# Performance work log

Hardware: AMD Instinct MI355X
Metric: run time of the kernel (lower is better)

Reference implementation:

```python
import jax, jax.numpy as jnp
import numpy as np

N_NODES = 100000
N_EDGES = 1600000
N_FEAT = 128
N_HID = 128
N_CLASS = 10
N_GRAPHS = 512
BN_EPS = 1e-5


def setup_inputs() -> dict:
    key = jax.random.key(0)
    ks = jax.random.split(key, 12)
    x = jax.random.normal(ks[0], (N_NODES, N_FEAT), dtype=jnp.float32)
    edge_index = jax.random.randint(ks[1], (2, N_EDGES), 0, N_NODES, dtype=jnp.int32)
    batch = jnp.sort(jax.random.randint(ks[2], (N_NODES,), 0, N_GRAPHS, dtype=jnp.int32))
    s1 = 1.0 / np.sqrt(N_FEAT)
    s2 = 1.0 / np.sqrt(N_HID)
    W1 = jax.random.uniform(ks[3], (N_FEAT, N_HID), jnp.float32, -s1, s1)
    b1 = jax.random.uniform(ks[4], (N_HID,), jnp.float32, -s1, s1)
    gamma = jnp.ones((N_HID,), jnp.float32)
    beta = jnp.zeros((N_HID,), jnp.float32)
    W2 = jax.random.uniform(ks[5], (N_HID, N_HID), jnp.float32, -s2, s2)
    b2 = jax.random.uniform(ks[6], (N_HID,), jnp.float32, -s2, s2)
    clsW = jax.random.uniform(ks[7], (N_HID, N_CLASS), jnp.float32, -s2, s2)
    clsb = jax.random.uniform(ks[8], (N_CLASS,), jnp.float32, -s2, s2)
    return {"x": x, "edge_index": edge_index, "batch": batch,
            "W1": W1, "b1": b1, "gamma": gamma, "beta": beta,
            "W2": W2, "b2": b2, "clsW": clsW, "clsb": clsb}


def _gcn_norm(edge_index, n_nodes):
    # add self-loops, compute symmetric normalization D^-1/2 A_hat D^-1/2
    loops = jnp.arange(n_nodes, dtype=edge_index.dtype)
    src = jnp.concatenate([edge_index[0], loops])
    dst = jnp.concatenate([edge_index[1], loops])
    deg = jax.ops.segment_sum(jnp.ones_like(dst, dtype=jnp.float32), dst,
                              num_segments=n_nodes)
    dinv = jnp.where(deg > 0, jax.lax.rsqrt(deg), 0.0)
    norm = dinv[src] * dinv[dst]  # [E + N]
    return src, dst, norm


def _gcn_conv(h, src, dst, norm, W, b, n_nodes):
    h = h @ W                                   # [N, nhid] dense GEMM
    msg = h[src] * norm[:, None]                # gather + scale  [E+N, nhid]
    out = jax.ops.segment_sum(msg, dst, num_segments=n_nodes)  # scatter-add
    return out + b


def reference(x, edge_index, batch, W1, b1, gamma, beta, W2, b2, clsW, clsb):
    n_nodes = x.shape[0]
    src, dst, norm = _gcn_norm(edge_index, n_nodes)
    # layer 1: GCNConv -> BatchNorm(eval, running stats 0/1) -> ReLU -> Dropout(eval=id)
    h = _gcn_conv(x, src, dst, norm, W1, b1, n_nodes)
    h = h * (gamma / jnp.sqrt(1.0 + BN_EPS)) + beta
    h = jax.nn.relu(h)
    # layer 2: GCNConv (output layer, no bn/act)
    h = _gcn_conv(h, src, dst, norm, W2, b2, n_nodes)
    # global mean pool over batch index
    sums = jax.ops.segment_sum(h, batch, num_segments=N_GRAPHS)          # [G, nhid]
    cnts = jax.ops.segment_sum(jnp.ones((n_nodes,), h.dtype), batch,
                               num_segments=N_GRAPHS)
    g = sums / jnp.maximum(cnts, 1.0)[:, None]
    out = jax.nn.log_softmax(g @ clsW + clsb, axis=1)                    # [G, nclass]
    return out, g
```

## Files before the change

### kernel.cpp

```cpp
#include <hip/hip_runtime.h>
#include <hip/hip_bf16.h>

#define N_NODES 100000
#define N_EDGES 1600000
#define N_FEAT 128
#define N_HID 128
#define N_CLASS 10
#define N_GRAPHS 512
#define BN_RSQRT 0.9999950000374997f

#define NRANGE 12500
#define NSUB 512
#define SCAP 640
#define HGROUP 32
#define BPB (NSUB / HGROUP)

typedef _Float16 half_t;
typedef __attribute__((ext_vector_type(2))) _Float16 half2v;
typedef __attribute__((ext_vector_type(4))) _Float16 half4v;
typedef __attribute__((ext_vector_type(8))) _Float16 half8v;
typedef __attribute__((ext_vector_type(4))) float floatx4;
typedef __attribute__((ext_vector_type(2))) float floatx2;

__global__ __launch_bounds__(256) void bucket_fused(
    const int* __restrict__ src, const int* __restrict__ dst,
    int* __restrict__ cnt, unsigned long long* __restrict__ bucketed,
    const float* __restrict__ W1, half_t* __restrict__ Wt1,
    const float* __restrict__ W2, half_t* __restrict__ Wt2,
    const int* __restrict__ batch, int* __restrict__ boffs,
    int chunkE, int E, int nnodes)
{
    __shared__ int wcnt[4][8];
    __shared__ int wbase[4][8];
    int blk = blockIdx.x;
    if (blk >= NSUB) {
        int k = blk - NSUB;
        if (k < 128) {
            int i = k * 256 + threadIdx.x;
            const float* W = (i < 16384) ? W1 : W2;
            half_t* Wt = (i < 16384) ? Wt1 : Wt2;
            int j = i & 16383;
            int c = j >> 7, kk = j & 127;
            Wt[(size_t)c * 128 + kk] = (half_t)W[(size_t)kk * 128 + c];
        } else {
            int i = (k - 128) * 256 + threadIdx.x;
            if (i < nnodes) {
                int b = batch[i];
                int prev = (i == 0) ? -1 : batch[i - 1];
                for (int g = prev + 1; g <= b; ++g) boffs[g] = i;
                if (i == nnodes - 1)
                    for (int g = b + 1; g <= N_GRAPHS; ++g) boffs[g] = nnodes;
            }
        }
        return;
    }
    int b = blk;
    int wave = threadIdx.x >> 6;
    int lane = threadIdx.x & 63;
    int e0 = b * chunkE;
    int e1 = e0 + chunkE < E ? e0 + chunkE : E;
    int iters = (chunkE + 255) / 256;

    int mycnt = 0;
    for (int it = 0; it < iters; ++it) {
        int e = e0 + it * 256 + threadIdx.x;
        bool valid = e < e1;
        int d = valid ? dst[e] : 0;
        int rr = (d * 8) / N_NODES;
#pragma unroll
        for (int r = 0; r < 8; ++r) {
            unsigned long long m = __ballot(valid && rr == r);
            if (lane == r) mycnt += __popcll(m);
        }
    }
    if (lane < 8) wcnt[wave][lane] = mycnt;
    __syncthreads();
    if (threadIdx.x < 8) {
        int r = threadIdx.x;
        int s = 0;
#pragma unroll
        for (int w = 0; w < 4; ++w) { wbase[w][r] = s; s += wcnt[w][r]; }
        cnt[r * NSUB + b] = s;
    }
    __syncthreads();

    int myoff = (lane < 8) ? wbase[wave][lane] : 0;
    for (int it = 0; it < iters; ++it) {
        int e = e0 + it * 256 + threadIdx.x;
        bool valid = e < e1;
        int s = valid ? src[e] : 0;
        int d = valid ? dst[e] : 0;
        int rr = (d * 8) / N_NODES;
        unsigned long long pk = ((unsigned long long)(unsigned)d << 32) | (unsigned)s;
#pragma unroll
        for (int r = 0; r < 8; ++r) {
            unsigned long long m = __ballot(valid && rr == r);
            int base_r = __shfl(myoff, r);
            if (valid && rr == r) {
                int pos = base_r + __popcll(m & ((1ull << lane) - 1));
                if (pos < SCAP)
                    bucketed[(size_t)(r * NSUB + b) * SCAP + pos] = pk;
            }
            if (lane == r) myoff += __popcll(m);
        }
    }
}

__global__ __launch_bounds__(256) void hist2(
    const unsigned long long* __restrict__ bucketed, const int* __restrict__ cnt,
    int* __restrict__ partial)
{
    __shared__ int h[NRANGE];
    int r = blockIdx.x & 7, g = blockIdx.x >> 3;
    for (int i = threadIdx.x; i < NRANGE; i += 256) h[i] = 0;
    __syncthreads();
    int rbase = r * NRANGE;
    for (int j = 0; j < BPB; ++j) {
        int b = g * BPB + j;
        int n = cnt[r * NSUB + b];
        if (n > SCAP) n = SCAP;
        const unsigned long long* seg = bucketed + (size_t)(r * NSUB + b) * SCAP;
        for (int i = threadIdx.x; i < n; i += 256)
            atomicAdd(&h[(int)(seg[i] >> 32) - rbase], 1);
    }
    __syncthreads();
    int* slice = partial + (size_t)(r * HGROUP + g) * NRANGE;
    for (int i = threadIdx.x; i < NRANGE; i += 256) slice[i] = h[i];
}

__global__ void deg_reduce(const int* __restrict__ partial, int* __restrict__ deg,
                           float* __restrict__ dinv, int* __restrict__ bsums, int n) {
    __shared__ int sm[256];
    int t = threadIdx.x;
    int i = blockIdx.x * 256 + t;
    int s = 0;
    if (i < n) {
        int rr = i / NRANGE;
        int dl = i - rr * NRANGE;
        const int* p = partial + (size_t)rr * HGROUP * NRANGE + dl;
#pragma unroll 8
        for (int g = 0; g < HGROUP; ++g) s += p[(size_t)g * NRANGE];
        deg[i] = s;
        dinv[i] = rsqrtf((float)s + 1.0f);
    }
    sm[t] = s;
    __syncthreads();
    for (int off = 128; off > 0; off >>= 1) {
        if (t < off) sm[t] += sm[t + off];
        __syncthreads();
    }
    if (t == 0) bsums[blockIdx.x] = sm[0];
}

__global__ void scan_small(int* __restrict__ bsums, int nb) {
    __shared__ int buf[1024];
    int t = threadIdx.x;
    int v = (t < nb) ? bsums[t] : 0;
    buf[t] = v;
    __syncthreads();
    for (int off = 1; off < 1024; off <<= 1) {
        int x = (t >= off) ? buf[t - off] : 0;
        __syncthreads();
        buf[t] += x;
        __syncthreads();
    }
    if (t < nb) bsums[t] = buf[t] - v;
}

__global__ __launch_bounds__(256) void scan_chunkoff_gemm1(
    const int* __restrict__ in, const int* __restrict__ bsums,
    int* __restrict__ rowptr, int* __restrict__ partial,
    int n, int total, int nb,
    const float* __restrict__ X, const half_t* __restrict__ Wt,
    const float* __restrict__ dinv, unsigned char* __restrict__ Y8, int nrows)
{
    __shared__ int s[256];
    if (blockIdx.x < (unsigned)nb) {
        int t = threadIdx.x;
        int i = blockIdx.x * 256 + t;
        int v = (i < n) ? in[i] : 0;
        s[t] = v;
        __syncthreads();
        for (int off = 1; off < 256; off <<= 1) {
            int x = (t >= off) ? s[t - off] : 0;
            __syncthreads();
            s[t] += x;
            __syncthreads();
        }
        if (i == 0) rowptr[n] = total;
        if (i < n) {
            int excl = bsums[blockIdx.x] + s[t] - v;
            rowptr[i] = excl;
            int rr = i / NRANGE;
            int dl = i - rr * NRANGE;
            int* p = partial + (size_t)rr * HGROUP * NRANGE + dl;
            int running = excl;
            for (int g = 0; g < HGROUP; ++g) {
                int tmp = p[(size_t)g * NRANGE];
                p[(size_t)g * NRANGE] = running;
                running += tmp;
            }
        }
        return;
    }
    int bb = blockIdx.x - nb;
    int wave = threadIdx.x >> 6;
    int lane = threadIdx.x & 63;
    int n16  = lane & 15;
    int quad = lane >> 4;
    int r0 = bb * 64 + wave * 16;
    if (r0 >= nrows) return;
    int row = r0 + n16;
    const float4* xrow = (const float4*)(X + (size_t)row * 128);
    half8v a[4];
#pragma unroll
    for (int kc = 0; kc < 4; ++kc) {
        float4 f0 = xrow[kc * 8 + quad * 2];
        float4 f1 = xrow[kc * 8 + quad * 2 + 1];
        half8v t = {(half_t)f0.x, (half_t)f0.y, (half_t)f0.z, (half_t)f0.w,
                    (half_t)f1.x, (half_t)f1.y, (half_t)f1.z, (half_t)f1.w};
        a[kc] = t;
    }
    float dr = dinv[row];
#pragma unroll
    for (int c = 0; c < 8; ++c) {
        const half8v* wrow = (const half8v*)(Wt + (size_t)(c * 16 + n16) * 128);
        floatx4 acc = {0.f, 0.f, 0.f, 0.f};
        acc = __builtin_amdgcn_mfma_f32_16x16x32_f16(wrow[0 * 4 + quad], a[0], acc, 0, 0, 0);
        acc = __builtin_amdgcn_mfma_f32_16x16x32_f16(wrow[1 * 4 + quad], a[1], acc, 0, 0, 0);
        acc = __builtin_amdgcn_mfma_f32_16x16x32_f16(wrow[2 * 4 + quad], a[2], acc, 0, 0, 0);
        acc = __builtin_amdgcn_mfma_f32_16x16x32_f16(wrow[3 * 4 + quad], a[3], acc, 0, 0, 0);
        int packed = __builtin_amdgcn_cvt_pk_fp8_f32(acc[0] * dr, acc[1] * dr, 0, false);
        packed = __builtin_amdgcn_cvt_pk_fp8_f32(acc[2] * dr, acc[3] * dr, packed, true);
        *(int*)(Y8 + (size_t)row * 128 + c * 16 + quad * 4) = packed;
    }
}

__global__ __launch_bounds__(256) void fill2(
    const unsigned long long* __restrict__ bucketed, const int* __restrict__ cnt,
    const int* __restrict__ partial, int* __restrict__ col)
{
    __shared__ int off[NRANGE];
    int r = blockIdx.x & 7, g = blockIdx.x >> 3;
    const int* slice = partial + (size_t)(r * HGROUP + g) * NRANGE;
    for (int i = threadIdx.x; i < NRANGE; i += 256) off[i] = slice[i];
    __syncthreads();
    int rbase = r * NRANGE;
    for (int j = 0; j < BPB; ++j) {
        int b = g * BPB + j;
        int n = cnt[r * NSUB + b];
        if (n > SCAP) n = SCAP;
        const unsigned long long* seg = bucketed + (size_t)(r * NSUB + b) * SCAP;
        for (int i = threadIdx.x; i < n; i += 256) {
            unsigned long long pk = seg[i];
            int pos = atomicAdd(&off[(int)(pk >> 32) - rbase], 1);
            col[pos] = (int)((unsigned)(pk & 0xffffffffu) << 7);
        }
    }
}

__global__ __launch_bounds__(256) void gemm2_mfma(
    const half_t* __restrict__ X, const half_t* __restrict__ Wt,
    const float* __restrict__ dinv, unsigned char* __restrict__ Y8, int nrows)
{
    int wave = threadIdx.x >> 6;
    int lane = threadIdx.x & 63;
    int n16  = lane & 15;
    int quad = lane >> 4;
    int r0 = blockIdx.x * 64 + wave * 16;
    if (r0 >= nrows) return;
    int row = r0 + n16;
    const half8v* xrow = (const half8v*)(X + (size_t)row * 128);
    half8v a0 = xrow[0 * 4 + quad];
    half8v a1 = xrow[1 * 4 + quad];
    half8v a2 = xrow[2 * 4 + quad];
    half8v a3 = xrow[3 * 4 + quad];
    float dr = dinv[row];
#pragma unroll
    for (int c = 0; c < 8; ++c) {
        const half8v* wrow = (const half8v*)(Wt + (size_t)(c * 16 + n16) * 128);
        floatx4 acc = {0.f, 0.f, 0.f, 0.f};
        acc = __builtin_amdgcn_mfma_f32_16x16x32_f16(wrow[0 * 4 + quad], a0, acc, 0, 0, 0);
        acc = __builtin_amdgcn_mfma_f32_16x16x32_f16(wrow[1 * 4 + quad], a1, acc, 0, 0, 0);
        acc = __builtin_amdgcn_mfma_f32_16x16x32_f16(wrow[2 * 4 + quad], a2, acc, 0, 0, 0);
        acc = __builtin_amdgcn_mfma_f32_16x16x32_f16(wrow[3 * 4 + quad], a3, acc, 0, 0, 0);
        int packed = __builtin_amdgcn_cvt_pk_fp8_f32(acc[0] * dr, acc[1] * dr, 0, false);
        packed = __builtin_amdgcn_cvt_pk_fp8_f32(acc[2] * dr, acc[3] * dr, packed, true);
        *(int*)(Y8 + (size_t)row * 128 + c * 16 + quad * 4) = packed;
    }
}

__global__ __launch_bounds__(256) void agg_fp8(
    const unsigned char* __restrict__ hs, half_t* __restrict__ out,
    const int* __restrict__ col, const int* __restrict__ rowptr,
    const float* __restrict__ bias,
    const float* __restrict__ gamma, const float* __restrict__ beta,
    int nnodes, int do_bn_relu)
{
    int wave = threadIdx.x >> 6;
    int lane = threadIdx.x & 63;
    int i = blockIdx.x * 4 + wave;
    if (i >= nnodes) return;
    unsigned f2 = (unsigned)lane << 1;
    unsigned ZOFF = (unsigned)nnodes << 7;

    int e0 = __builtin_amdgcn_readfirstlane(rowptr[i]);
    int e1 = __builtin_amdgcn_readfirstlane(rowptr[i + 1]);

    unsigned short us = *(const unsigned short*)(hs + (((unsigned)i << 7) | f2));

    floatx2 acc0 = {0.f, 0.f}, acc1 = {0.f, 0.f};
    for (int base = e0; base < e1; base += 16) {
        int idx = base + (lane & 15);
        unsigned cv = (idx < e1) ? (unsigned)col[idx] : ZOFF;
#pragma unroll
        for (int k = 0; k < 16; k += 2) {
            unsigned sa = (unsigned)__builtin_amdgcn_readlane((int)cv, k);
            unsigned sb = (unsigned)__builtin_amdgcn_readlane((int)cv, k + 1);
            unsigned short ua = *(const unsigned short*)(hs + (sa | f2));
            unsigned short ub = *(const unsigned short*)(hs + (sb | f2));
            acc0 += __builtin_amdgcn_cvt_pk_f32_fp8((int)(unsigned)ua, false);
            acc1 += __builtin_amdgcn_cvt_pk_f32_fp8((int)(unsigned)ub, false);
        }
    }
    floatx2 acc = acc0 + acc1;
    acc += __builtin_amdgcn_cvt_pk_f32_fp8((int)(unsigned)us, false);

    float di = rsqrtf((float)(e1 - e0) + 1.0f);
    float2 bi = *(const float2*)(bias + 2 * lane);
    float o0 = fmaf(di, acc.x, bi.x);
    float o1 = fmaf(di, acc.y, bi.y);
    if (do_bn_relu) {
        float2 ga = *(const float2*)(gamma + 2 * lane);
        float2 be = *(const float2*)(beta + 2 * lane);
        o0 = fmaf(o0, ga.x * BN_RSQRT, be.x);
        o1 = fmaf(o1, ga.y * BN_RSQRT, be.y);
        o0 = o0 > 0.f ? o0 : 0.f;
        o1 = o1 > 0.f ? o1 : 0.f;
    }
    half2v ov = {(half_t)o0, (half_t)o1};
    *(half2v*)(out + (size_t)i * 128 + 2 * lane) = ov;
}

__global__ __launch_bounds__(512) void pool_cls(
    const half_t* __restrict__ h, const int* __restrict__ boffs,
    const float* __restrict__ clsW, const float* __restrict__ clsb,
    float* __restrict__ gout, float* __restrict__ out)
{
    __shared__ float red[8][128];
    __shared__ float zbuf[16];
    int g = blockIdx.x;
    int w = threadIdx.x >> 6;
    int lane = threadIdx.x & 63;
    int n0 = boffs[g], n1 = boffs[g + 1];
    float ax = 0.f, ay = 0.f;
    for (int n = n0 + w; n < n1; n += 8) {
        half2v v = *(const half2v*)(h + (size_t)n * 128 + lane * 2);
        ax += (float)v.x;
        ay += (float)v.y;
    }
    red[w][lane * 2] = ax;
    red[w][lane * 2 + 1] = ay;
    __syncthreads();
    if (w == 0) {
        float sx = 0.f, sy = 0.f;
#pragma unroll
        for (int j = 0; j < 8; ++j) {
            sx += red[j][lane * 2];
            sy += red[j][lane * 2 + 1];
        }
        float cnt = (float)((n1 - n0) > 1 ? (n1 - n0) : 1);
        float g0 = sx / cnt, g1 = sy / cnt;
        gout[(size_t)g * 128 + lane * 2] = g0;
        gout[(size_t)g * 128 + lane * 2 + 1] = g1;
        red[0][lane * 2] = g0;
        red[0][lane * 2 + 1] = g1;
    }
    __syncthreads();
    if (threadIdx.x < N_CLASS) {
        int c = threadIdx.x;
        float z = clsb[c];
        for (int k = 0; k < N_HID; ++k)
            z = fmaf(red[0][k], clsW[k * N_CLASS + c], z);
        zbuf[c] = z;
    }
    __syncthreads();
    if (threadIdx.x == 0) {
        float m = zbuf[0];
#pragma unroll
        for (int c = 1; c < N_CLASS; ++c) m = fmaxf(m, zbuf[c]);
        float s = 0.f;
#pragma unroll
        for (int c = 0; c < N_CLASS; ++c) s += expf(zbuf[c] - m);
        float l = logf(s);
#pragma unroll
        for (int c = 0; c < N_CLASS; ++c)
            out[(size_t)g * N_CLASS + c] = zbuf[c] - m - l;
    }
}

extern "C" void kernel_launch(void* const* d_in, const int* in_sizes, int n_in,
                              void* d_out, int out_size, void* d_ws, size_t ws_size,
                              hipStream_t stream) {
    const float* x     = (const float*)d_in[0];
    const int*   ei    = (const int*)d_in[1];
    const int*   batch = (const int*)d_in[2];
    const float* W1    = (const float*)d_in[3];
    const float* b1    = (const float*)d_in[4];
    const float* gamma = (const float*)d_in[5];
    const float* beta  = (const float*)d_in[6];
    const float* W2    = (const float*)d_in[7];
    const float* b2    = (const float*)d_in[8];
    const float* clsW  = (const float*)d_in[9];
    const float* clsb  = (const float*)d_in[10];

    const int N = in_sizes[0] / N_FEAT;
    const int E = in_sizes[1] / 2;
    const int* src = ei;
    const int* dst = ei + E;

    unsigned char* BA8 = (unsigned char*)d_ws;
    half_t* BB = (half_t*)(BA8 + (size_t)(N + 1) * 128);
    half_t* Wt1 = BB + (size_t)N * 128;
    half_t* Wt2 = Wt1 + 16384;
    int*   col     = (int*)(Wt2 + 16384);
    int*   rowptr  = col + E;
    int*   deg     = rowptr + (N + 4);
    float* dinv    = (float*)(deg + N);
    int*   cnt     = (int*)(dinv + N);
    unsigned long long* bucketed =
        (unsigned long long*)(cnt + 8 * NSUB);
    int*   partial = (int*)(bucketed + (size_t)8 * NSUB * SCAP);
    int*   boffs   = partial + 8 * HGROUP * NRANGE;
    int*   bsums   = boffs + N_GRAPHS + 4;

    const int nb = (N + 255) / 256;
    const int chunkE = (E + NSUB - 1) / NSUB;
    const int gemmBlocks = (N + 63) / 64;

    hipMemsetAsync(BA8 + (size_t)N * 128, 0, 128, stream);

    bucket_fused<<<NSUB + 128 + nb, 256, 0, stream>>>(
        src, dst, cnt, bucketed, W1, Wt1, W2, Wt2, batch, boffs, chunkE, E, N);
    hist2<<<8 * HGROUP, 256, 0, stream>>>(bucketed, cnt, partial);
    deg_reduce<<<nb, 256, 0, stream>>>(partial, deg, dinv, bsums, N);
    scan_small<<<1, 1024, 0, stream>>>(bsums, nb);
    scan_chunkoff_gemm1<<<nb + gemmBlocks, 256, 0, stream>>>(
        deg, bsums, rowptr, partial, N, E, nb, x, Wt1, dinv, BA8, N);
    fill2<<<256, 256, 0, stream>>>(bucketed, cnt, partial, col);
    agg_fp8<<<(N + 3) / 4, 256, 0, stream>>>(BA8, BB, col, rowptr, b1, gamma, beta, N, 1);
    gemm2_mfma<<<gemmBlocks, 256, 0, stream>>>(BB, Wt2, dinv, BA8, N);
    agg_fp8<<<(N + 3) / 4, 256, 0, stream>>>(BA8, BB, col, rowptr, b2, gamma, beta, N, 0);

    float* out = (float*)d_out;
    float* gsec = out + (size_t)N_GRAPHS * N_CLASS;
    pool_cls<<<N_GRAPHS, 512, 0, stream>>>(BB, boffs, clsW, clsb, gsec, out);
}
```

Before: 329.9 us.

## Aggregate four nodes per wave with 8-byte fp8 gathers; batch partial-scan loads

The SpMM aggregation kernel now handles four destination nodes per wave instead of one. Each 16-lane quarter owns one node and gathers 8 fp8 features per lane with 64-bit loads. Neighbor indices are broadcast with readlane and selected per quarter, so each gather instruction now fetches rows from four nodes at once. This raises memory-level parallelism and cuts per-node instruction overhead, but a wave loops for the maximum degree among its four nodes, so imbalanced degrees waste lanes. Separately, the per-row chunk-offset scan in the scan kernel now loads all 32 partial values up front before the serial prefix update, exposing more load concurrency.

```diff
diff --git a/kernel.cpp b/kernel.cpp
--- a/kernel.cpp
+++ b/kernel.cpp
@@ -194,9 +194,13 @@
             int rr = i / NRANGE;
             int dl = i - rr * NRANGE;
             int* p = partial + (size_t)rr * HGROUP * NRANGE + dl;
+            int vals[32];
+#pragma unroll
+            for (int g = 0; g < 32; ++g) vals[g] = p[(size_t)g * NRANGE];
             int running = excl;
-            for (int g = 0; g < HGROUP; ++g) {
-                int tmp = p[(size_t)g * NRANGE];
+#pragma unroll
+            for (int g = 0; g < 32; ++g) {
+                int tmp = vals[g];
                 p[(size_t)g * NRANGE] = running;
                 running += tmp;
             }
@@ -299,47 +303,92 @@
 {
     int wave = threadIdx.x >> 6;
     int lane = threadIdx.x & 63;
-    int i = blockIdx.x * 4 + wave;
-    if (i >= nnodes) return;
-    unsigned f2 = (unsigned)lane << 1;
+    int q = lane >> 4;
+    int l16 = lane & 15;
+    int nb4 = (blockIdx.x * 4 + wave) * 4;
+    int i = nb4 + q;
+    bool valid = i < nnodes;
+    unsigned iq = valid ? (unsigned)i : (unsigned)nnodes;
+    unsigned f8 = (unsigned)l16 << 3;
     unsigned ZOFF = (unsigned)nnodes << 7;
 
-    int e0 = __builtin_amdgcn_readfirstlane(rowptr[i]);
-    int e1 = __builtin_amdgcn_readfirstlane(rowptr[i + 1]);
-
-    unsigned short us = *(const unsigned short*)(hs + (((unsigned)i << 7) | f2));
-
-    floatx2 acc0 = {0.f, 0.f}, acc1 = {0.f, 0.f};
-    for (int base = e0; base < e1; base += 16) {
-        int idx = base + (lane & 15);
+    int e0 = valid ? rowptr[i] : 0;
+    int e1 = valid ? rowptr[i + 1] : 0;
+    int deg = e1 - e0;
+    int m = deg;
+    m = max(m, __shfl_xor(m, 16));
+    m = max(m, __shfl_xor(m, 32));
+    int nchunk = (m + 15) >> 4;
+
+    unsigned long long us = *(const unsigned long long*)(hs + ((iq << 7) | f8));
+
+    floatx2 a0 = {0.f, 0.f}, a1 = {0.f, 0.f}, a2 = {0.f, 0.f}, a3 = {0.f, 0.f};
+    for (int t = 0; t < nchunk; ++t) {
+        int idx = e0 + t * 16 + l16;
         unsigned cv = (idx < e1) ? (unsigned)col[idx] : ZOFF;
 #pragma unroll
-        for (int k = 0; k < 16; k += 2) {
-            unsigned sa = (unsigned)__builtin_amdgcn_readlane((int)cv, k);
-            unsigned sb = (unsigned)__builtin_amdgcn_readlane((int)cv, k + 1);
-            unsigned short ua = *(const unsigned short*)(hs + (sa | f2));
-            unsigned short ub = *(const unsigned short*)(hs + (sb | f2));
-            acc0 += __builtin_amdgcn_cvt_pk_f32_fp8((int)(unsigned)ua, false);
-            acc1 += __builtin_amdgcn_cvt_pk_f32_fp8((int)(unsigned)ub, false);
-        }
-    }
-    floatx2 acc = acc0 + acc1;
-    acc += __builtin_amdgcn_cvt_pk_f32_fp8((int)(unsigned)us, false);
-
-    float di = rsqrtf((float)(e1 - e0) + 1.0f);
-    float2 bi = *(const float2*)(bias + 2 * lane);
-    float o0 = fmaf(di, acc.x, bi.x);
-    float o1 = fmaf(di, acc.y, bi.y);
+        for (int k = 0; k < 16; ++k) {
+            unsigned sA = (unsigned)__builtin_amdgcn_readlane((int)cv, k);
+            unsigned sB = (unsigned)__builtin_amdgcn_readlane((int)cv, k + 16);
+            unsigned sC = (unsigned)__builtin_amdgcn_readlane((int)cv, k + 32);
+            unsigned sD = (unsigned)__builtin_amdgcn_readlane((int)cv, k + 48);
+            unsigned rAB = (q & 1) ? sB : sA;
+            unsigned rCD = (q & 1) ? sD : sC;
+            unsigned r = (q & 2) ? rCD : rAB;
+            unsigned long long v = *(const unsigned long long*)(hs + (r | f8));
+            unsigned lo = (unsigned)v, hi = (unsigned)(v >> 32);
+            a0 += __builtin_amdgcn_cvt_pk_f32_fp8((int)lo, false);
+            a1 += __builtin_amdgcn_cvt_pk_f32_fp8((int)lo, true);
+            a2 += __builtin_amdgcn_cvt_pk_f32_fp8((int)hi, false);
+            a3 += __builtin_amdgcn_cvt_pk_f32_fp8((int)hi, true);
+        }
+    }
+    {
+        unsigned lo = (unsigned)us, hi = (unsigned)(us >> 32);
+        a0 += __builtin_amdgcn_cvt_pk_f32_fp8((int)lo, false);
+        a1 += __builtin_amdgcn_cvt_pk_f32_fp8((int)lo, true);
+        a2 += __builtin_amdgcn_cvt_pk_f32_fp8((int)hi, false);
+        a3 += __builtin_amdgcn_cvt_pk_f32_fp8((int)hi, true);
+    }
+
+    if (!valid) return;
+    float di = rsqrtf((float)deg + 1.0f);
+    int fbase = l16 * 8;
+    float4 bi0 = *(const float4*)(bias + fbase);
+    float4 bi1 = *(const float4*)(bias + fbase + 4);
+    float o0 = fmaf(di, a0.x, bi0.x);
+    float o1 = fmaf(di, a0.y, bi0.y);
+    float o2 = fmaf(di, a1.x, bi0.z);
+    float o3 = fmaf(di, a1.y, bi0.w);
+    float o4 = fmaf(di, a2.x, bi1.x);
+    float o5 = fmaf(di, a2.y, bi1.y);
+    float o6 = fmaf(di, a3.x, bi1.z);
+    float o7 = fmaf(di, a3.y, bi1.w);
     if (do_bn_relu) {
-        float2 ga = *(const float2*)(gamma + 2 * lane);
-        float2 be = *(const float2*)(beta + 2 * lane);
-        o0 = fmaf(o0, ga.x * BN_RSQRT, be.x);
-        o1 = fmaf(o1, ga.y * BN_RSQRT, be.y);
+        float4 ga0 = *(const float4*)(gamma + fbase);
+        float4 ga1 = *(const float4*)(gamma + fbase + 4);
+        float4 be0 = *(const float4*)(beta + fbase);
+        float4 be1 = *(const float4*)(beta + fbase + 4);
+        o0 = fmaf(o0, ga0.x * BN_RSQRT, be0.x);
+        o1 = fmaf(o1, ga0.y * BN_RSQRT, be0.y);
+        o2 = fmaf(o2, ga0.z * BN_RSQRT, be0.z);
+        o3 = fmaf(o3, ga0.w * BN_RSQRT, be0.w);
+        o4 = fmaf(o4, ga1.x * BN_RSQRT, be1.x);
+        o5 = fmaf(o5, ga1.y * BN_RSQRT, be1.y);
+        o6 = fmaf(o6, ga1.z * BN_RSQRT, be1.z);
+        o7 = fmaf(o7, ga1.w * BN_RSQRT, be1.w);
         o0 = o0 > 0.f ? o0 : 0.f;
         o1 = o1 > 0.f ? o1 : 0.f;
-    }
-    half2v ov = {(half_t)o0, (half_t)o1};
-    *(half2v*)(out + (size_t)i * 128 + 2 * lane) = ov;
+        o2 = o2 > 0.f ? o2 : 0.f;
+        o3 = o3 > 0.f ? o3 : 0.f;
+        o4 = o4 > 0.f ? o4 : 0.f;
+        o5 = o5 > 0.f ? o5 : 0.f;
+        o6 = o6 > 0.f ? o6 : 0.f;
+        o7 = o7 > 0.f ? o7 : 0.f;
+    }
+    half8v ov = {(half_t)o0, (half_t)o1, (half_t)o2, (half_t)o3,
+                 (half_t)o4, (half_t)o5, (half_t)o6, (half_t)o7};
+    *(half8v*)(out + (size_t)i * 128 + fbase) = ov;
 }
 
 __global__ __launch_bounds__(512) void pool_cls(
@@ -437,6 +486,7 @@
     const int nb = (N + 255) / 256;
     const int chunkE = (E + NSUB - 1) / NSUB;
     const int gemmBlocks = (N + 63) / 64;
+    const int aggBlocks = (N + 15) / 16;
 
     hipMemsetAsync(BA8 + (size_t)N * 128, 0, 128, stream);
 
@@ -448,9 +498,9 @@
     scan_chunkoff_gemm1<<<nb + gemmBlocks, 256, 0, stream>>>(
         deg, bsums, rowptr, partial, N, E, nb, x, Wt1, dinv, BA8, N);
     fill2<<<256, 256, 0, stream>>>(bucketed, cnt, partial, col);
-    agg_fp8<<<(N + 3) / 4, 256, 0, stream>>>(BA8, BB, col, rowptr, b1, gamma, beta, N, 1);
+    agg_fp8<<<aggBlocks, 256, 0, stream>>>(BA8, BB, col, rowptr, b1, gamma, beta, N, 1);
     gemm2_mfma<<<gemmBlocks, 256, 0, stream>>>(BB, Wt2, dinv, BA8, N);
-    agg_fp8<<<(N + 3) / 4, 256, 0, stream>>>(BA8, BB, col, rowptr, b2, gamma, beta, N, 0);
+    agg_fp8<<<aggBlocks, 256, 0, stream>>>(BA8, BB, col, rowptr, b2, gamma, beta, N, 0);
 
     float* out = (float*)d_out;
     float* gsec = out + (size_t)N_GRAPHS * N_CLASS;
```

Result: faster. 319.3 us (-3.2%).
